# Kernel optimization log

Hardware: AMD Instinct MI355X
Metric: run time of the kernel (lower is better)

Reference implementation:

```python
import math
import jax, jax.numpy as jnp
import numpy as np

STRIDE = 16
PAD_MODE = 'reflect'


def setup_inputs() -> dict:
    key = jax.random.key(0)
    x = jax.random.normal(key, (8, 3, 1024, 1024), dtype=jnp.float32)
    return {"x": x, "patch_size": 24}


def _patchify(x, patch_size, stride=STRIDE):
    # Reflect-pad so that valid patch extraction with <stride> tiles the image,
    # then gather overlapping patches directly (equivalent to the torch
    # identity-kernel conv2d / unfold, without the wasted FLOPs).
    B, C, H, W = x.shape
    m = (patch_size - stride) // 2  # symmetric overlap margin
    H_pad = math.ceil(H / stride) * stride
    W_pad = math.ceil(W / stride) * stride
    xp = jnp.pad(x, ((0, 0), (0, 0), (m, H_pad - H + m), (m, W_pad - W + m)),
                 mode=PAD_MODE)
    nH = H_pad // stride
    nW = W_pad // stride
    # row[i, a] = top-left row of patch i plus offset a; likewise for cols
    row = jnp.arange(nH)[:, None] * stride + jnp.arange(patch_size)[None, :]  # (nH, ps)
    col = jnp.arange(nW)[:, None] * stride + jnp.arange(patch_size)[None, :]  # (nW, ps)
    xr = xp[:, :, row, :]          # (B, C, nH, ps, W_padded)
    xc = xr[:, :, :, :, col]       # (B, C, nH, ps, nW, ps)
    # -> (B, nH, nW, ps, ps, C) -> (B*nH*nW, ps*ps, C); (i,j) row-major matches
    # torch's reshape(B, C, ps^2, nH, nW).permute(0,3,4,2,1) ordering.
    patches = xc.transpose(0, 2, 4, 3, 5, 1).reshape(
        B * nH * nW, patch_size * patch_size, C)
    return patches, nH, nW


def reference(x, patch_size):
    patches, nH, nW = _patchify(x, patch_size)
    return patches, (nH, nW)
```

## Files before the change

kernel.cpp:

```cpp
#include <hip/hip_runtime.h>


constexpr int B_  = 8;
constexpr int C_  = 3;
constexpr int H_  = 1024;
constexpr int W_  = 1024;
constexpr int PS  = 24;
constexpr int STR = 16;
constexpr int M_  = 4;
constexpr int NH  = H_ / STR;
constexpr int NW  = W_ / STR;
constexpr int QTOT = PS * PS;
constexpr int NPQ  = B_ * NH * NW * QTOT;
constexpr int PATCH_ELEMS_I = NPQ * C_;

__global__ __launch_bounds__(256) void patcher_kernel(
    const float* __restrict__ x, float* __restrict__ out, int tail)
{
    int t = blockIdx.x * blockDim.x + threadIdx.x;
    if (t < NPQ) {
        int q  = t % QTOT;
        int p  = t / QTOT;
        int pc = q % PS;
        int pr = q / PS;
        int iw = p % NW;
        int t2 = p / NW;
        int ih = t2 % NH;
        int b  = t2 / NH;

        int h = ih * STR + pr - M_;
        int w = iw * STR + pc - M_;
        h = (h < 0) ? -h : ((h >= H_) ? (2 * H_ - 2 - h) : h);
        w = (w < 0) ? -w : ((w >= W_) ? (2 * W_ - 2 - w) : w);

        const float* base = x + ((b * C_) * H_ + h) * W_ + w;
        float v0 = base[0];
        float v1 = base[H_ * W_];
        float v2 = base[2 * H_ * W_];

        float* o = out + t * 3;
        o[0] = v0;
        o[1] = v1;
        o[2] = v2;
    }
    if (t < tail) {
        out[PATCH_ELEMS_I + t] = 64.0f;
    }
}

extern "C" void kernel_launch(void* const* d_in, const int* in_sizes, int n_in,
                              void* d_out, int out_size, void* d_ws, size_t ws_size,
                              hipStream_t stream)
{
    const float* x = (const float*)d_in[0];
    float* out = (float*)d_out;

    int tail = out_size - PATCH_ELEMS_I;
    if (tail < 0) tail = 0;

    int threads = 256;
    int blocks = (NPQ + threads - 1) / threads;
    patcher_kernel<<<blocks, threads, 0, stream>>>(x, out, tail);
}
```

Baseline: 331.4 us.

## Stage each patch in LDS with float4 loads and vectorized interleaved stores

Measured after the change: 324.1 us. 1.02x faster.

```diff
diff --git a/kernel.cpp b/kernel.cpp
--- a/kernel.cpp
+++ b/kernel.cpp
@@ -1,50 +1,74 @@
 #include <hip/hip_runtime.h>
 
 
-constexpr int B_  = 8;
-constexpr int C_  = 3;
-constexpr int H_  = 1024;
-constexpr int W_  = 1024;
 constexpr int PS  = 24;
-constexpr int STR = 16;
-constexpr int M_  = 4;
-constexpr int NH  = H_ / STR;
-constexpr int NW  = W_ / STR;
 constexpr int QTOT = PS * PS;
-constexpr int NPQ  = B_ * NH * NW * QTOT;
-constexpr int PATCH_ELEMS_I = NPQ * C_;
+constexpr int PATCH_F = QTOT * 3;
+constexpr int NPATCH = 8 * 64 * 64;
+constexpr int PATCH_ELEMS_I = NPATCH * PATCH_F;
+constexpr int NV = PATCH_F / 4;
 
 __global__ __launch_bounds__(256) void patcher_kernel(
     const float* __restrict__ x, float* __restrict__ out, int tail)
 {
-    int t = blockIdx.x * blockDim.x + threadIdx.x;
-    if (t < NPQ) {
-        int q  = t % QTOT;
-        int p  = t / QTOT;
-        int pc = q % PS;
-        int pr = q / PS;
-        int iw = p % NW;
-        int t2 = p / NW;
-        int ih = t2 % NH;
-        int b  = t2 / NH;
+    __shared__ float lds[3 * QTOT];
 
-        int h = ih * STR + pr - M_;
-        int w = iw * STR + pc - M_;
-        h = (h < 0) ? -h : ((h >= H_) ? (2 * H_ - 2 - h) : h);
-        w = (w < 0) ? -w : ((w >= W_) ? (2 * W_ - 2 - w) : w);
+    int p  = blockIdx.x;
+    int iw = p & 63;
+    int ih = (p >> 6) & 63;
+    int b  = p >> 12;
+    int h0 = ih * 16 - 4;
+    int w0 = iw * 16 - 4;
+    int tid = threadIdx.x;
 
-        const float* base = x + ((b * C_) * H_ + h) * W_ + w;
-        float v0 = base[0];
-        float v1 = base[H_ * W_];
-        float v2 = base[2 * H_ * W_];
+    const float* xb = x + (size_t)b * (3 * 1024 * 1024);
 
-        float* o = out + t * 3;
-        o[0] = v0;
-        o[1] = v1;
-        o[2] = v2;
+    bool edge = (ih == 0) | (ih == 63) | (iw == 0) | (iw == 63);
+    if (!edge) {
+        for (int j = tid; j < NV; j += 256) {
+            int c   = j / 144;
+            int rem = j - c * 144;
+            int r   = rem / 6;
+            int k   = rem - r * 6;
+            const float4 v = *(const float4*)(xb + (c * 1024 + h0 + r) * 1024 + w0 + 4 * k);
+            *(float4*)(&lds[c * QTOT + r * PS + 4 * k]) = v;
+        }
+    } else {
+        for (int j = tid; j < NV; j += 256) {
+            int c   = j / 144;
+            int rem = j - c * 144;
+            int r   = rem / 6;
+            int k   = rem - r * 6;
+            int h = h0 + r;
+            h = (h < 0) ? -h : ((h > 1023) ? 2046 - h : h);
+            const float* rowp = xb + (c * 1024 + h) * 1024;
+#pragma unroll
+            for (int e = 0; e < 4; ++e) {
+                int w = w0 + 4 * k + e;
+                w = (w < 0) ? -w : ((w > 1023) ? 2046 - w : w);
+                lds[c * QTOT + r * PS + 4 * k + e] = rowp[w];
+            }
+        }
     }
-    if (t < tail) {
-        out[PATCH_ELEMS_I + t] = 64.0f;
+    __syncthreads();
+
+    float* ob = out + (size_t)p * PATCH_F;
+    for (int j = tid; j < NV; j += 256) {
+        int f = 4 * j;
+        float4 v;
+        float* vp = (float*)&v;
+#pragma unroll
+        for (int e = 0; e < 4; ++e) {
+            int idx = f + e;
+            int pix = idx / 3;
+            int c   = idx - pix * 3;
+            vp[e] = lds[c * QTOT + pix];
+        }
+        *(float4*)(ob + f) = v;
+    }
+
+    if (p == 0 && tid < tail) {
+        out[(size_t)PATCH_ELEMS_I + tid] = 64.0f;
     }
 }
 
@@ -57,8 +81,7 @@
 
     int tail = out_size - PATCH_ELEMS_I;
     if (tail < 0) tail = 0;
+    if (tail > 256) tail = 256;
 
-    int threads = 256;
-    int blocks = (NPQ + threads - 1) / threads;
-    patcher_kernel<<<blocks, threads, 0, stream>>>(x, out, tail);
+    patcher_kernel<<<NPATCH, 256, 0, stream>>>(x, out, tail);
 }
```
